# Performance work log

Measured on AMD Instinct MI355X. Metric: run time of the kernel, lower is better.

Reference implementation:

```python
import jax, jax.numpy as jnp
import numpy as np

IGNORE_LABEL_ID = -100
GRID = 40                 # grid_width
PATH = 6                  # path_token_id
SP_W = 10.0               # spatial_penalty_weight
CONN_W = 5.0              # connectivity_weight
SEQ = GRID * GRID         # 1600
BIG = SEQ                 # sentinel larger than any flat index


def _spatial_penalty(pred):
    """Vectorized version of spatial_connectivity_loss's per-batch python loop.
    For each predicted path token, find the NEXT path token in flat order and
    penalize Manhattan jumps > 1. pred: [B, SEQ] int."""
    B = pred.shape[0]
    mask = pred == PATH                                   # [B,S]
    idx = jnp.arange(SEQ, dtype=jnp.int32)
    cand = jnp.where(mask, idx[None, :], BIG)
    # nxt[b,i] = smallest path index >= i (reverse cumulative min)
    nxt = jax.lax.cummin(cand, axis=1, reverse=True)
    # next path index strictly after i
    nxt_after = jnp.concatenate([nxt[:, 1:], jnp.full((B, 1), BIG, nxt.dtype)], axis=1)
    valid = mask & (nxt_after < BIG)                      # pairs (i, next)
    p2 = jnp.minimum(nxt_after, SEQ - 1)                  # keep indices in-range
    r1, c1 = idx // GRID, idx % GRID
    r2, c2 = p2 // GRID, p2 % GRID
    dist = jnp.abs(r1[None, :] - r2) + jnp.abs(c1[None, :] - c2)
    pen = jnp.where(valid & (dist > 1), (dist - 1).astype(jnp.float32) * SP_W, 0.0)
    return pen.sum() / B


def _connectivity_penalty(pred):
    """Parallel connected-component labeling (min-label propagation) replacing
    the CPU flood fill. pred: [B, SEQ] int."""
    B = pred.shape[0]
    mask = pred.reshape(B, GRID, GRID) == PATH
    idx = jnp.arange(SEQ, dtype=jnp.int32).reshape(GRID, GRID)
    lab0 = jnp.where(mask, idx[None], BIG)

    def prop(lab):
        p = jnp.pad(lab, ((0, 0), (1, 1), (1, 1)), constant_values=BIG)
        nmin = jnp.minimum(jnp.minimum(p[:, :-2, 1:-1], p[:, 2:, 1:-1]),
                           jnp.minimum(p[:, 1:-1, :-2], p[:, 1:-1, 2:]))
        return jnp.where(mask, jnp.minimum(lab, nmin), BIG)

    def cond(st):
        return st[1]

    def body(st):
        lab, _ = st
        new = prop(lab)
        return (new, jnp.any(new != lab))

    lab, _ = jax.lax.while_loop(cond, body, (lab0, jnp.array(True)))
    # a component is counted once at its minimal (root) cell
    comp = (mask & (lab == idx[None])).sum(axis=(1, 2))
    pen = jnp.where(comp > 1, (comp - 1).astype(jnp.float32) * CONN_W, 0.0)
    return pen.sum() / B


def setup_inputs() -> dict:
    key = jax.random.key(0)
    k1, k2, k3, k4, k5 = jax.random.split(key, 5)
    B, S, V = 1024, SEQ, 32
    return {
        "logits": jax.random.normal(k1, (B, S, V), dtype=jnp.float32),
        "labels": jax.random.randint(k2, (B, S), 0, V).astype(jnp.int64),
        "q_halt_logits": jax.random.normal(k3, (B,), dtype=jnp.float32),
        "halted": jax.random.randint(k4, (B,), 0, 2).astype(bool),
        "steps": jax.random.randint(k5, (B,), 0, 16).astype(jnp.int32),
    }


def reference(logits, labels, q_halt_logits, halted, steps):
    # halted/steps feed no-grad metrics only; loss math below matches ACTLossHead.
    mask = labels != IGNORE_LABEL_ID                       # [B,S]
    loss_counts = mask.sum(-1)
    loss_divisor = jnp.maximum(loss_counts, 1)[:, None].astype(logits.dtype)

    pred = jnp.argmax(logits, axis=-1)                     # [B,S]
    is_correct = mask & (pred == labels)
    seq_is_correct = is_correct.sum(-1) == loss_counts     # [B] bool

    # softmax cross entropy with ignore_index, per token
    logp = jax.nn.log_softmax(logits, axis=-1)
    safe_labels = jnp.maximum(labels, 0)
    ce = -jnp.take_along_axis(logp, safe_labels[..., None], axis=-1)[..., 0]
    ce = jnp.where(mask, ce, 0.0)
    lm_loss = (ce / loss_divisor).sum()

    # BCE-with-logits, reduction='sum'
    t = seq_is_correct.astype(logits.dtype)
    x = q_halt_logits
    q_halt_loss = (jnp.maximum(x, 0) - x * t + jnp.log1p(jnp.exp(-jnp.abs(x)))).sum()

    spatial_loss = _spatial_penalty(pred)
    connectivity_loss = _connectivity_penalty(pred)

    total_loss = lm_loss + 0.5 * q_halt_loss + spatial_loss + connectivity_loss
    return total_loss
```

## Files before the change

kernel.cpp:

```cpp
#include <hip/hip_runtime.h>
#include <cstdint>

#define GRIDW   40
#define SEQ     1600
#define NVOCAB  32
#define PATH_ID 6
#define IGNORE_ID (-100)
#define NWORDS  25
#define BLK     256

__global__ __launch_bounds__(BLK) void act_loss_kernel(
    const float* __restrict__ logits,
    const int*   __restrict__ labels,
    const float* __restrict__ qhalt,
    float*       __restrict__ out,
    int B)
{
    const int b   = blockIdx.x;
    const int tid = threadIdx.x;

    __shared__ uint8_t  path[SEQ];
    __shared__ uint16_t lab[SEQ];
    __shared__ uint16_t pos[SEQ];
    __shared__ uint64_t words[NWORDS];
    __shared__ int      offs[NWORDS + 1];
    __shared__ int      npath_s;
    __shared__ float    red_f[BLK];
    __shared__ int      red_i[BLK];
    __shared__ int      red_j[BLK];
    __shared__ int      changed;
    __shared__ float    part_a;

    float ce_sum = 0.0f;
    int   cnt = 0, cor = 0;

    const float* base  = logits + (size_t)b * SEQ * NVOCAB;
    const int*   lbase = labels + (size_t)b * SEQ;

    for (int i = tid; i < SEQ; i += BLK) {
        const float4* p4 = (const float4*)(base + (size_t)i * NVOCAB);
        float x[NVOCAB];
#pragma unroll
        for (int j = 0; j < 8; ++j) {
            float4 v = p4[j];
            x[4*j+0] = v.x; x[4*j+1] = v.y; x[4*j+2] = v.z; x[4*j+3] = v.w;
        }
        int lbl = lbase[i];

        float m = x[0]; int arg = 0;
#pragma unroll
        for (int j = 1; j < NVOCAB; ++j) {
            if (x[j] > m) { m = x[j]; arg = j; }
        }
        float s = 0.0f;
#pragma unroll
        for (int j = 0; j < NVOCAB; ++j) s += __expf(x[j] - m);
        float lse = m + __logf(s);

        bool msk  = (lbl != IGNORE_ID);
        int  slbl = (lbl < 0) ? 0 : lbl;
        float xl = 0.0f;
#pragma unroll
        for (int j = 0; j < NVOCAB; ++j) xl = (j == slbl) ? x[j] : xl;

        ce_sum += msk ? (lse - xl) : 0.0f;
        cnt    += msk ? 1 : 0;
        cor    += (msk && arg == lbl) ? 1 : 0;
        path[i] = (arg == PATH_ID) ? 1 : 0;
    }
    __syncthreads();

    red_f[tid] = ce_sum; red_i[tid] = cnt; red_j[tid] = cor;
    __syncthreads();
    for (int s = BLK / 2; s > 0; s >>= 1) {
        if (tid < s) {
            red_f[tid] += red_f[tid + s];
            red_i[tid] += red_i[tid + s];
            red_j[tid] += red_j[tid + s];
        }
        __syncthreads();
    }
    if (tid == 0) {
        float ce_tot = red_f[0];
        int   c_tot  = red_i[0];
        int   k_tot  = red_j[0];
        float lm = ce_tot / (float)max(c_tot, 1);
        float t  = (k_tot == c_tot) ? 1.0f : 0.0f;
        float xq = qhalt[b];
        float bce = fmaxf(xq, 0.0f) - xq * t + log1pf(expf(-fabsf(xq)));
        part_a = lm + 0.5f * bce;
    }
    __syncthreads();

    if (tid < NWORDS) {
        uint64_t w = 0;
        int basei = tid * 64;
#pragma unroll 8
        for (int k = 0; k < 64; ++k)
            w |= ((uint64_t)path[basei + k]) << k;
        words[tid] = w;
    }
    __syncthreads();
    if (tid == 0) {
        int o = 0;
        for (int t2 = 0; t2 < NWORDS; ++t2) { offs[t2] = o; o += __popcll(words[t2]); }
        offs[NWORDS] = o;
        npath_s = o;
    }
    __syncthreads();
    if (tid < NWORDS) {
        int o = offs[tid];
        uint64_t w = words[tid];
        int basei = tid * 64;
        while (w) {
            int k = __ffsll((unsigned long long)w) - 1;
            pos[o++] = (uint16_t)(basei + k);
            w &= (w - 1);
        }
    }
    __syncthreads();

    const int np = npath_s;
    int sp_units = 0;
    for (int q = tid; q + 1 < np; q += BLK) {
        int i = pos[q], j = pos[q + 1];
        int dist = abs(i / GRIDW - j / GRIDW) + abs(i % GRIDW - j % GRIDW);
        if (dist > 1) sp_units += dist - 1;
    }

    for (int i = tid; i < SEQ; i += BLK)
        lab[i] = path[i] ? (uint16_t)i : (uint16_t)0xFFFF;
    __syncthreads();

    for (;;) {
        if (tid == 0) changed = 0;
        __syncthreads();
        int local = 0;
        for (int i = tid; i < SEQ; i += BLK) {
            if (!path[i]) continue;
            int r = i / GRIDW, c = i % GRIDW;
            uint16_t v = lab[i];
            uint16_t nm = v;
            if (r > 0)          { uint16_t u = lab[i - GRIDW]; nm = (u < nm) ? u : nm; }
            if (r < GRIDW - 1)  { uint16_t u = lab[i + GRIDW]; nm = (u < nm) ? u : nm; }
            if (c > 0)          { uint16_t u = lab[i - 1];     nm = (u < nm) ? u : nm; }
            if (c < GRIDW - 1)  { uint16_t u = lab[i + 1];     nm = (u < nm) ? u : nm; }
            if (nm < v) { lab[i] = nm; local = 1; }
        }
        if (local) changed = 1;
        __syncthreads();
        if (!changed) break;
    }

    int comp = 0;
    for (int i = tid; i < SEQ; i += BLK)
        comp += (path[i] && lab[i] == (uint16_t)i) ? 1 : 0;

    red_i[tid] = sp_units; red_j[tid] = comp;
    __syncthreads();
    for (int s = BLK / 2; s > 0; s >>= 1) {
        if (tid < s) {
            red_i[tid] += red_i[tid + s];
            red_j[tid] += red_j[tid + s];
        }
        __syncthreads();
    }

    if (tid == 0) {
        int sp_tot   = red_i[0];
        int comp_tot = red_j[0];
        int conn_units = (comp_tot > 1) ? (comp_tot - 1) : 0;
        float total = part_a +
                      ((float)sp_tot * 10.0f + (float)conn_units * 5.0f) / (float)B;
        atomicAdd(out, total);
    }
}

extern "C" void kernel_launch(void* const* d_in, const int* in_sizes, int n_in,
                              void* d_out, int out_size, void* d_ws, size_t ws_size,
                              hipStream_t stream) {
    const float* logits = (const float*)d_in[0];
    const int*   labels = (const int*)d_in[1];
    const float* qhalt  = (const float*)d_in[2];
    float* out = (float*)d_out;
    const int B = in_sizes[2];

    hipMemsetAsync(out, 0, (size_t)out_size * sizeof(float), stream);
    act_loss_kernel<<<dim3(B), dim3(BLK), 0, stream>>>(logits, labels, qhalt, out, B);
}
```

Before: 307.7 us.

## Split token work across 8 lanes and use wave-level ballot/shuffle reductions

Each token's 32 logits are now handled by 8 lanes, each loading one float4, with max, argmax, sum-exp and label lookup combined through shuffles. This gives coalesced loads and less per-thread register pressure. The path bitmask is built with __ballot, the prefix offsets with a wave scan, and the block reductions with shuffles plus a 4-entry shared array. The label-propagation loop uses __syncthreads_count, which removes the shared changed flag and one barrier per iteration. The cost is extra shuffle traffic and 7 of every 8 lanes sitting idle during the per-token bookkeeping.

```diff
diff --git a/kernel.cpp b/kernel.cpp
--- a/kernel.cpp
+++ b/kernel.cpp
@@ -8,6 +8,7 @@
 #define IGNORE_ID (-100)
 #define NWORDS  25
 #define BLK     256
+#define NWAVES  (BLK / 64)
 
 __global__ __launch_bounds__(BLK) void act_loss_kernel(
     const float* __restrict__ logits,
@@ -16,8 +17,11 @@
     float*       __restrict__ out,
     int B)
 {
-    const int b   = blockIdx.x;
-    const int tid = threadIdx.x;
+    const int b    = blockIdx.x;
+    const int tid  = threadIdx.x;
+    const int lane = tid & 63;
+    const int wid  = tid >> 6;
+    const int sub  = tid & 7;
 
     __shared__ uint8_t  path[SEQ];
     __shared__ uint16_t lab[SEQ];
@@ -25,10 +29,9 @@
     __shared__ uint64_t words[NWORDS];
     __shared__ int      offs[NWORDS + 1];
     __shared__ int      npath_s;
-    __shared__ float    red_f[BLK];
-    __shared__ int      red_i[BLK];
-    __shared__ int      red_j[BLK];
-    __shared__ int      changed;
+    __shared__ float    wr_f[NWAVES];
+    __shared__ int      wr_i[NWAVES];
+    __shared__ int      wr_j[NWAVES];
     __shared__ float    part_a;
 
     float ce_sum = 0.0f;
@@ -37,77 +40,88 @@
     const float* base  = logits + (size_t)b * SEQ * NVOCAB;
     const int*   lbase = labels + (size_t)b * SEQ;
 
-    for (int i = tid; i < SEQ; i += BLK) {
-        const float4* p4 = (const float4*)(base + (size_t)i * NVOCAB);
-        float x[NVOCAB];
-#pragma unroll
-        for (int j = 0; j < 8; ++j) {
-            float4 v = p4[j];
-            x[4*j+0] = v.x; x[4*j+1] = v.y; x[4*j+2] = v.z; x[4*j+3] = v.w;
-        }
-        int lbl = lbase[i];
+    const int tokOff = tid >> 3;
+    for (int i0 = 0; i0 < SEQ; i0 += BLK / 8) {
+        const int tok = i0 + tokOff;
+        float4 v = ((const float4*)(base + (size_t)tok * NVOCAB))[sub];
+        int lbl = lbase[tok];
 
-        float m = x[0]; int arg = 0;
-#pragma unroll
-        for (int j = 1; j < NVOCAB; ++j) {
-            if (x[j] > m) { m = x[j]; arg = j; }
-        }
-        float s = 0.0f;
-#pragma unroll
-        for (int j = 0; j < NVOCAB; ++j) s += __expf(x[j] - m);
-        float lse = m + __logf(s);
+        float m = v.x;
+        if (v.y > m) m = v.y;
+        if (v.z > m) m = v.z;
+        if (v.w > m) m = v.w;
+        for (int d = 1; d < 8; d <<= 1)
+            m = fmaxf(m, __shfl_xor(m, d));
+        int cand = 999;
+        if (v.w == m) cand = 4 * sub + 3;
+        if (v.z == m) cand = 4 * sub + 2;
+        if (v.y == m) cand = 4 * sub + 1;
+        if (v.x == m) cand = 4 * sub + 0;
+        for (int d = 1; d < 8; d <<= 1)
+            cand = min(cand, __shfl_xor(cand, d));
+
+        float s = __expf(v.x - m) + __expf(v.y - m)
+                + __expf(v.z - m) + __expf(v.w - m);
+        for (int d = 1; d < 8; d <<= 1)
+            s += __shfl_xor(s, d);
 
         bool msk  = (lbl != IGNORE_ID);
         int  slbl = (lbl < 0) ? 0 : lbl;
-        float xl = 0.0f;
-#pragma unroll
-        for (int j = 0; j < NVOCAB; ++j) xl = (j == slbl) ? x[j] : xl;
+        int   k2    = slbl & 3;
+        float xcand = (k2 == 0) ? v.x : (k2 == 1) ? v.y : (k2 == 2) ? v.z : v.w;
+        int   owner = (lane & ~7) | ((slbl >> 2) & 7);
+        float xl    = __shfl(xcand, owner);
 
-        ce_sum += msk ? (lse - xl) : 0.0f;
-        cnt    += msk ? 1 : 0;
-        cor    += (msk && arg == lbl) ? 1 : 0;
-        path[i] = (arg == PATH_ID) ? 1 : 0;
+        if (sub == 0) {
+            float lse = m + __logf(s);
+            ce_sum += msk ? (lse - xl) : 0.0f;
+            cnt    += msk ? 1 : 0;
+            cor    += (msk && cand == lbl) ? 1 : 0;
+            path[tok] = (cand == PATH_ID) ? 1 : 0;
+        }
     }
     __syncthreads();
 
-    red_f[tid] = ce_sum; red_i[tid] = cnt; red_j[tid] = cor;
+    for (int basei = 0; basei < SEQ; basei += BLK) {
+        int idx = basei + tid;
+        bool p = (idx < SEQ) ? (path[idx] != 0) : false;
+        uint64_t w = __ballot(p);
+        int widx = (basei >> 6) + wid;
+        if (lane == 0 && widx < NWORDS) words[widx] = w;
+    }
+
+    for (int d = 1; d < 64; d <<= 1) {
+        ce_sum += __shfl_xor(ce_sum, d);
+        cnt    += __shfl_xor(cnt, d);
+        cor    += __shfl_xor(cor, d);
+    }
+    if (lane == 0) { wr_f[wid] = ce_sum; wr_i[wid] = cnt; wr_j[wid] = cor; }
     __syncthreads();
-    for (int s = BLK / 2; s > 0; s >>= 1) {
-        if (tid < s) {
-            red_f[tid] += red_f[tid + s];
-            red_i[tid] += red_i[tid + s];
-            red_j[tid] += red_j[tid + s];
-        }
-        __syncthreads();
-    }
+
     if (tid == 0) {
-        float ce_tot = red_f[0];
-        int   c_tot  = red_i[0];
-        int   k_tot  = red_j[0];
+        float ce_tot = wr_f[0] + wr_f[1] + wr_f[2] + wr_f[3];
+        int   c_tot  = wr_i[0] + wr_i[1] + wr_i[2] + wr_i[3];
+        int   k_tot  = wr_j[0] + wr_j[1] + wr_j[2] + wr_j[3];
         float lm = ce_tot / (float)max(c_tot, 1);
         float t  = (k_tot == c_tot) ? 1.0f : 0.0f;
         float xq = qhalt[b];
         float bce = fmaxf(xq, 0.0f) - xq * t + log1pf(expf(-fabsf(xq)));
         part_a = lm + 0.5f * bce;
     }
+
+    if (wid == 0) {
+        uint64_t w = (lane < NWORDS) ? words[lane] : 0ull;
+        int pc = __popcll(w);
+        int c = pc;
+        for (int d = 1; d < 32; d <<= 1) {
+            int t = __shfl_up(c, d);
+            if (lane >= d) c += t;
+        }
+        if (lane < NWORDS) offs[lane] = c - pc;
+        if (lane == NWORDS - 1) { offs[NWORDS] = c; npath_s = c; }
+    }
     __syncthreads();
 
-    if (tid < NWORDS) {
-        uint64_t w = 0;
-        int basei = tid * 64;
-#pragma unroll 8
-        for (int k = 0; k < 64; ++k)
-            w |= ((uint64_t)path[basei + k]) << k;
-        words[tid] = w;
-    }
-    __syncthreads();
-    if (tid == 0) {
-        int o = 0;
-        for (int t2 = 0; t2 < NWORDS; ++t2) { offs[t2] = o; o += __popcll(words[t2]); }
-        offs[NWORDS] = o;
-        npath_s = o;
-    }
-    __syncthreads();
     if (tid < NWORDS) {
         int o = offs[tid];
         uint64_t w = words[tid];
@@ -133,42 +147,35 @@
     __syncthreads();
 
     for (;;) {
-        if (tid == 0) changed = 0;
-        __syncthreads();
         int local = 0;
         for (int i = tid; i < SEQ; i += BLK) {
             if (!path[i]) continue;
             int r = i / GRIDW, c = i % GRIDW;
             uint16_t v = lab[i];
             uint16_t nm = v;
-            if (r > 0)          { uint16_t u = lab[i - GRIDW]; nm = (u < nm) ? u : nm; }
-            if (r < GRIDW - 1)  { uint16_t u = lab[i + GRIDW]; nm = (u < nm) ? u : nm; }
-            if (c > 0)          { uint16_t u = lab[i - 1];     nm = (u < nm) ? u : nm; }
-            if (c < GRIDW - 1)  { uint16_t u = lab[i + 1];     nm = (u < nm) ? u : nm; }
+            if (r > 0)         { uint16_t u = lab[i - GRIDW]; nm = (u < nm) ? u : nm; }
+            if (r < GRIDW - 1) { uint16_t u = lab[i + GRIDW]; nm = (u < nm) ? u : nm; }
+            if (c > 0)         { uint16_t u = lab[i - 1];     nm = (u < nm) ? u : nm; }
+            if (c < GRIDW - 1) { uint16_t u = lab[i + 1];     nm = (u < nm) ? u : nm; }
             if (nm < v) { lab[i] = nm; local = 1; }
         }
-        if (local) changed = 1;
-        __syncthreads();
-        if (!changed) break;
+        if (__syncthreads_count(local) == 0) break;
     }
 
     int comp = 0;
     for (int i = tid; i < SEQ; i += BLK)
         comp += (path[i] && lab[i] == (uint16_t)i) ? 1 : 0;
 
-    red_i[tid] = sp_units; red_j[tid] = comp;
+    for (int d = 1; d < 64; d <<= 1) {
+        sp_units += __shfl_xor(sp_units, d);
+        comp     += __shfl_xor(comp, d);
+    }
+    if (lane == 0) { wr_i[wid] = sp_units; wr_j[wid] = comp; }
     __syncthreads();
-    for (int s = BLK / 2; s > 0; s >>= 1) {
-        if (tid < s) {
-            red_i[tid] += red_i[tid + s];
-            red_j[tid] += red_j[tid + s];
-        }
-        __syncthreads();
-    }
 
     if (tid == 0) {
-        int sp_tot   = red_i[0];
-        int comp_tot = red_j[0];
+        int sp_tot   = wr_i[0] + wr_i[1] + wr_i[2] + wr_i[3];
+        int comp_tot = wr_j[0] + wr_j[1] + wr_j[2] + wr_j[3];
         int conn_units = (comp_tot > 1) ? (comp_tot - 1) : 0;
         float total = part_a +
                       ((float)sp_tot * 10.0f + (float)conn_units * 5.0f) / (float)B;
```

Result: slower. 326.5 us (+6.1%).
